# Kernel tuning notes

Hardware: AMD Instinct MI355X
Metric: run time of the kernel (lower is better)

## Reference

```python
import math
import jax, jax.numpy as jnp
import numpy as np

B, M, L, H = 8, 2048, 2048, 1024


def setup_inputs() -> dict:
    key = jax.random.key(0)
    k1, k2, k3, k4 = jax.random.split(key, 4)
    return {
        "query": jax.random.normal(k1, (B, M, H), dtype=jnp.float32),
        "key": jax.random.normal(k2, (B, L, H), dtype=jnp.float32),
        "value": jax.random.normal(k3, (B, L, H), dtype=jnp.float32),
        "key_pe": jax.random.normal(k4, (1, H, L), dtype=jnp.float32),
        "hidden_size": H,
    }


def reference(query, key, value, key_pe, hidden_size):
    # content scores: [B, M, L]
    attn_cont = jnp.einsum("bmh,blh->bml", query, key)
    # relative-position scores: [B, M, H] @ [1, H, L] -> [B, M, L]
    attn_pos = jnp.matmul(query, key_pe)
    # NOTE: the original module computes softmax(attn)+dropout but then
    # (as written) multiplies VALUE by the raw content scores, not the
    # softmaxed attention. We reproduce that math faithfully; the softmax
    # is dead code w.r.t. the output (kept here for documentation, DCE'd by jit).
    attn = jax.nn.softmax((attn_cont + attn_pos) / math.sqrt(hidden_size), axis=-1)  # noqa: F841
    # dropout: identity in eval mode (and unused for the output anyway)
    out = jnp.matmul(attn_cont, value)  # [B, M, H]
    return out
```

## Files before the change

kernel.cpp:

```cpp
#include <hip/hip_runtime.h>
#include <hip/hip_bf16.h>


typedef __bf16 bf16x8 __attribute__((ext_vector_type(8)));
typedef float f32x4 __attribute__((ext_vector_type(4)));
typedef unsigned short u16_t;

#define GLD_LDS16(g, l)                                                        \
  __builtin_amdgcn_global_load_lds(                                            \
      (const __attribute__((address_space(1))) void*)(g),                      \
      (__attribute__((address_space(3))) void*)(l), 16, 0, 0)

static __device__ inline u16_t f2b(float x) {
  __hip_bfloat16 h = __float2bfloat16(x);
  u16_t u;
  __builtin_memcpy(&u, &h, 2);
  return u;
}

__global__ __launch_bounds__(256) void cvt_f32_bf16(
    const float* __restrict__ in, u16_t* __restrict__ out, size_t n8) {
  const size_t i = (size_t)blockIdx.x * 256 + threadIdx.x;
  if (i >= n8) return;
  const float4 a = *(const float4*)(in + i * 8);
  const float4 b = *(const float4*)(in + i * 8 + 4);
  u16_t v[8] = {f2b(a.x), f2b(a.y), f2b(a.z), f2b(a.w),
                f2b(b.x), f2b(b.y), f2b(b.z), f2b(b.w)};
  *(uint4*)(out + i * 8) = *(const uint4*)v;
}

__global__ __launch_bounds__(256) void transpose_cvt(
    const float* __restrict__ in, u16_t* __restrict__ out, int L, int Hd) {
  __shared__ u16_t tile[64 * 65];
  in  += (size_t)blockIdx.z * (size_t)L * Hd;
  out += (size_t)blockIdx.z * (size_t)L * Hd;
  const int h0 = blockIdx.x * 64;
  const int l0 = blockIdx.y * 64;

  const int c4 = (threadIdx.x & 15) * 4;
  const int r0 = threadIdx.x >> 4;
#pragma unroll
  for (int it = 0; it < 4; ++it) {
    const int r = r0 + 16 * it;
    const float4 f = *(const float4*)(in + (size_t)(l0 + r) * Hd + h0 + c4);
    tile[(c4 + 0) * 65 + r] = f2b(f.x);
    tile[(c4 + 1) * 65 + r] = f2b(f.y);
    tile[(c4 + 2) * 65 + r] = f2b(f.z);
    tile[(c4 + 3) * 65 + r] = f2b(f.w);
  }
  __syncthreads();

  const int c8 = (threadIdx.x & 7) * 8;
  const int rr = threadIdx.x >> 3;
#pragma unroll
  for (int it = 0; it < 2; ++it) {
    const int r = rr + 32 * it;
    u16_t p[8];
#pragma unroll
    for (int u = 0; u < 8; ++u) p[u] = tile[r * 65 + c8 + u];
    *(uint4*)(out + (size_t)(h0 + r) * L + l0 + c8) = *(const uint4*)p;
  }
}

static __device__ inline void store_c(float* p, float v) { *p = v; }
static __device__ inline void store_c(u16_t* p, float v) { *p = f2b(v); }

template <typename OutT>
__global__ __launch_bounds__(256) void gemm_bt_128(
    const u16_t* __restrict__ A, const u16_t* __restrict__ Bt,
    OutT* __restrict__ C, int M, int N, int K, long sA, long sB, long sC) {
  __shared__ __align__(16) u16_t As[128 * 32];
  __shared__ __align__(16) u16_t Bs[128 * 32];

  A  += (size_t)blockIdx.z * (size_t)sA;
  Bt += (size_t)blockIdx.z * (size_t)sB;
  C  += (size_t)blockIdx.z * (size_t)sC;

  const int tid = threadIdx.x;
  const int m0 = blockIdx.y * 128;
  const int n0 = blockIdx.x * 128;

  const int lane = tid & 63;
  const int w  = tid >> 6;
  const int wm = w & 1;
  const int wn = w >> 1;
  const int s  = lane & 15;
  const int q  = lane >> 4;

  const int i0 = tid, i1 = tid + 256;
  const u16_t* gA0 = A  + (size_t)(m0 + (i0 >> 2)) * K + (i0 & 3) * 8;
  const u16_t* gA1 = A  + (size_t)(m0 + (i1 >> 2)) * K + (i1 & 3) * 8;
  const u16_t* gB0 = Bt + (size_t)(n0 + (i0 >> 2)) * K + (i0 & 3) * 8;
  const u16_t* gB1 = Bt + (size_t)(n0 + (i1 >> 2)) * K + (i1 & 3) * 8;
  u16_t* lA0 = As + i0 * 8;
  u16_t* lA1 = As + i1 * 8;
  u16_t* lB0 = Bs + i0 * 8;
  u16_t* lB1 = Bs + i1 * 8;

  f32x4 acc[4][4];
#pragma unroll
  for (int r = 0; r < 4; ++r)
#pragma unroll
    for (int c = 0; c < 4; ++c) acc[r][c] = (f32x4){0.f, 0.f, 0.f, 0.f};

  for (int k0 = 0; k0 < K; k0 += 32) {
    GLD_LDS16(gA0 + k0, lA0);
    GLD_LDS16(gA1 + k0, lA1);
    GLD_LDS16(gB0 + k0, lB0);
    GLD_LDS16(gB1 + k0, lB1);
    __syncthreads();

    bf16x8 af[4], bfr[4];
#pragma unroll
    for (int r = 0; r < 4; ++r)
      af[r] = *(const bf16x8*)(As + (64 * wm + 16 * r + s) * 32 + q * 8);
#pragma unroll
    for (int c = 0; c < 4; ++c)
      bfr[c] = *(const bf16x8*)(Bs + (64 * wn + 16 * c + s) * 32 + q * 8);
#pragma unroll
    for (int r = 0; r < 4; ++r)
#pragma unroll
      for (int c = 0; c < 4; ++c)
        acc[r][c] = __builtin_amdgcn_mfma_f32_16x16x32_bf16(af[r], bfr[c],
                                                            acc[r][c], 0, 0, 0);
    __syncthreads();
  }

#pragma unroll
  for (int r = 0; r < 4; ++r) {
#pragma unroll
    for (int c = 0; c < 4; ++c) {
      const int col = n0 + 64 * wn + 16 * c + s;
#pragma unroll
      for (int e = 0; e < 4; ++e) {
        const int row = m0 + 64 * wm + 16 * r + q * 4 + e;
        store_c(&C[(size_t)row * N + col], acc[r][c][e]);
      }
    }
  }
}

extern "C" void kernel_launch(void* const* d_in, const int* in_sizes, int n_in,
                              void* d_out, int out_size, void* d_ws, size_t ws_size,
                              hipStream_t stream) {
  const int B = 8, M = 2048, L = 2048, H = 1024;

  const float* q = (const float*)d_in[0];
  const float* k = (const float*)d_in[1];
  const float* v = (const float*)d_in[2];

  const size_t nKt = (size_t)B * H * L;
  const size_t nQ  = (size_t)B * M * H;
  const size_t nW  = (size_t)B * H * H;
  const size_t need = (2 * nKt + nQ + nW) * sizeof(u16_t);
  if (ws_size < need) return;

  u16_t* Kt = (u16_t*)d_ws;
  u16_t* Vt = Kt + nKt;
  u16_t* Qb = Vt + nKt;
  u16_t* W  = Qb + nQ;

  dim3 tb(256);

  cvt_f32_bf16<<<dim3((unsigned)(nQ / 8 / 256)), tb, 0, stream>>>(q, Qb, nQ / 8);

  dim3 tg(H / 64, L / 64, B);
  transpose_cvt<<<tg, tb, 0, stream>>>(k, Kt, L, H);
  transpose_cvt<<<tg, tb, 0, stream>>>(v, Vt, L, H);

  dim3 g1(H / 128, H / 128, B);
  gemm_bt_128<u16_t><<<g1, tb, 0, stream>>>(Vt, Kt, W, H, H, L,
                                            (long)H * L, (long)H * L, (long)H * H);

  dim3 g2(H / 128, M / 128, B);
  gemm_bt_128<float><<<g2, tb, 0, stream>>>(Qb, W, (float*)d_out, M, H, H,
                                            (long)M * H, (long)H * H, (long)M * H);
}
```

Before: 344.2 us.

## Double GEMM K-tile to 64, XOR-swizzle LDS, interleave batches in grid

Both bf16 GEMMs now stage 64-wide K tiles instead of 32, which halves the number of barrier pairs per K loop and gives each LDS stage more MFMA work. Global-to-LDS copies place 16-byte chunks with an XOR swizzle on the row index, and the fragment reads undo it, to avoid LDS bank conflicts on the row-strided reads. The 3D grid is flattened so consecutive blocks cycle through batches first, changing the order tiles are scheduled in and therefore their L2 reuse. The trade-off is double the LDS per block (32 KB) and more address registers, which may lower occupancy.

```diff
diff --git a/kernel.cpp b/kernel.cpp
--- a/kernel.cpp
+++ b/kernel.cpp
@@ -69,17 +69,19 @@
 __global__ __launch_bounds__(256) void gemm_bt_128(
     const u16_t* __restrict__ A, const u16_t* __restrict__ Bt,
     OutT* __restrict__ C, int M, int N, int K, long sA, long sB, long sC) {
-  __shared__ __align__(16) u16_t As[128 * 32];
-  __shared__ __align__(16) u16_t Bs[128 * 32];
+  __shared__ __align__(16) u16_t As[128 * 64];
+  __shared__ __align__(16) u16_t Bs[128 * 64];
 
-  A  += (size_t)blockIdx.z * (size_t)sA;
-  Bt += (size_t)blockIdx.z * (size_t)sB;
-  C  += (size_t)blockIdx.z * (size_t)sC;
+  const int batch = blockIdx.x & 7;
+  const int t = blockIdx.x >> 3;
+  const int m0 = (t >> 3) * 128;
+  const int n0 = (t & 7) * 128;
+
+  A  += (size_t)batch * (size_t)sA;
+  Bt += (size_t)batch * (size_t)sB;
+  C  += (size_t)batch * (size_t)sC;
 
   const int tid = threadIdx.x;
-  const int m0 = blockIdx.y * 128;
-  const int n0 = blockIdx.x * 128;
-
   const int lane = tid & 63;
   const int w  = tid >> 6;
   const int wm = w & 1;
@@ -87,15 +89,20 @@
   const int s  = lane & 15;
   const int q  = lane >> 4;
 
-  const int i0 = tid, i1 = tid + 256;
-  const u16_t* gA0 = A  + (size_t)(m0 + (i0 >> 2)) * K + (i0 & 3) * 8;
-  const u16_t* gA1 = A  + (size_t)(m0 + (i1 >> 2)) * K + (i1 & 3) * 8;
-  const u16_t* gB0 = Bt + (size_t)(n0 + (i0 >> 2)) * K + (i0 & 3) * 8;
-  const u16_t* gB1 = Bt + (size_t)(n0 + (i1 >> 2)) * K + (i1 & 3) * 8;
-  u16_t* lA0 = As + i0 * 8;
-  u16_t* lA1 = As + i1 * 8;
-  u16_t* lB0 = Bs + i0 * 8;
-  u16_t* lB1 = Bs + i1 * 8;
+  const u16_t* gA[4];
+  const u16_t* gB[4];
+  u16_t* lA[4];
+  u16_t* lB[4];
+#pragma unroll
+  for (int j = 0; j < 4; ++j) {
+    const int i = tid + 256 * j;
+    const int row = i >> 3;
+    const int gchunk = (i & 7) ^ (row & 7);
+    gA[j] = A  + (size_t)(m0 + row) * K + gchunk * 8;
+    gB[j] = Bt + (size_t)(n0 + row) * K + gchunk * 8;
+    lA[j] = As + i * 8;
+    lB[j] = Bs + i * 8;
+  }
 
   f32x4 acc[4][4];
 #pragma unroll
@@ -103,26 +110,33 @@
 #pragma unroll
     for (int c = 0; c < 4; ++c) acc[r][c] = (f32x4){0.f, 0.f, 0.f, 0.f};
 
-  for (int k0 = 0; k0 < K; k0 += 32) {
-    GLD_LDS16(gA0 + k0, lA0);
-    GLD_LDS16(gA1 + k0, lA1);
-    GLD_LDS16(gB0 + k0, lB0);
-    GLD_LDS16(gB1 + k0, lB1);
+  const int s7 = s & 7;
+
+  for (int k0 = 0; k0 < K; k0 += 64) {
+#pragma unroll
+    for (int j = 0; j < 4; ++j) {
+      GLD_LDS16(gA[j] + k0, lA[j]);
+      GLD_LDS16(gB[j] + k0, lB[j]);
+    }
     __syncthreads();
 
-    bf16x8 af[4], bfr[4];
 #pragma unroll
-    for (int r = 0; r < 4; ++r)
-      af[r] = *(const bf16x8*)(As + (64 * wm + 16 * r + s) * 32 + q * 8);
+    for (int kk = 0; kk < 2; ++kk) {
+      const int slot = (kk * 4 + q) ^ s7;
+      bf16x8 af[4], bfr[4];
 #pragma unroll
-    for (int c = 0; c < 4; ++c)
-      bfr[c] = *(const bf16x8*)(Bs + (64 * wn + 16 * c + s) * 32 + q * 8);
-#pragma unroll
-    for (int r = 0; r < 4; ++r)
+      for (int r = 0; r < 4; ++r)
+        af[r] = *(const bf16x8*)(As + (64 * wm + 16 * r + s) * 64 + slot * 8);
 #pragma unroll
       for (int c = 0; c < 4; ++c)
-        acc[r][c] = __builtin_amdgcn_mfma_f32_16x16x32_bf16(af[r], bfr[c],
-                                                            acc[r][c], 0, 0, 0);
+        bfr[c] = *(const bf16x8*)(Bs + (64 * wn + 16 * c + s) * 64 + slot * 8);
+#pragma unroll
+      for (int r = 0; r < 4; ++r)
+#pragma unroll
+        for (int c = 0; c < 4; ++c)
+          acc[r][c] = __builtin_amdgcn_mfma_f32_16x16x32_bf16(af[r], bfr[c],
+                                                              acc[r][c], 0, 0, 0);
+    }
     __syncthreads();
   }
 
@@ -168,11 +182,9 @@
   transpose_cvt<<<tg, tb, 0, stream>>>(k, Kt, L, H);
   transpose_cvt<<<tg, tb, 0, stream>>>(v, Vt, L, H);
 
-  dim3 g1(H / 128, H / 128, B);
-  gemm_bt_128<u16_t><<<g1, tb, 0, stream>>>(Vt, Kt, W, H, H, L,
-                                            (long)H * L, (long)H * L, (long)H * H);
+  gemm_bt_128<u16_t><<<dim3(B * (H / 128) * (H / 128)), tb, 0, stream>>>(
+      Vt, Kt, W, H, H, L, (long)H * L, (long)H * L, (long)H * H);
 
-  dim3 g2(H / 128, M / 128, B);
-  gemm_bt_128<float><<<g2, tb, 0, stream>>>(Qb, W, (float*)d_out, M, H, H,
-                                            (long)M * H, (long)H * H, (long)M * H);
+  gemm_bt_128<float><<<dim3(B * (M / 128) * (H / 128)), tb, 0, stream>>>(
+      Qb, W, (float*)d_out, M, H, H, (long)M * H, (long)H * H, (long)M * H);
 }
```

Measured after the change: 315.1 us. -8.5%, faster.
